# Optimization experiments

Hardware: AMD Instinct MI355X
Metric: run time of the kernel (lower is better)

Reference implementation:

```python
import jax, jax.numpy as jnp
import numpy as np

NUM_NOD = 6
MAX_PREV = 5
NUM_EDGE = 20  # (1+5)*5//2 + 5*(6-5)
D = 1024
H = 8
LN_EPS = 1e-6


def setup_inputs() -> dict:
    key = jax.random.key(0)
    ks = jax.random.split(key, 12)
    B, S = 8, 1024
    scale = 1.0 / np.sqrt(D)
    return {
        "inputs": jax.random.normal(ks[0], (B, S, D), jnp.float32),
        "ew": jax.random.uniform(ks[1], (NUM_NOD, 3), jnp.float32),
        "act_w": jax.random.uniform(ks[2], (NUM_NOD,), jnp.float32),
        "We": jax.random.normal(ks[3], (NUM_EDGE, D, D), jnp.float32) * scale,
        "be": jnp.zeros((NUM_EDGE, D), jnp.float32),
        "Wq": jax.random.normal(ks[4], (NUM_NOD, D, D), jnp.float32) * scale,
        "Wk": jax.random.normal(ks[5], (NUM_NOD, D, D), jnp.float32) * scale,
        "Wv": jax.random.normal(ks[6], (NUM_NOD, D, D), jnp.float32) * scale,
        "Wo": jax.random.normal(ks[7], (NUM_NOD, D, D), jnp.float32) * scale,
        "ln_g": jnp.ones((D,), jnp.float32),
        "ln_b": jnp.zeros((D,), jnp.float32),
    }


def _layernorm(x, g, b):
    mu = jnp.mean(x, axis=-1, keepdims=True)
    var = jnp.mean(jnp.square(x - mu), axis=-1, keepdims=True)
    return (x - mu) * jax.lax.rsqrt(var + LN_EPS) * g + b


def _mha(q, k, v, wq, wk, wv, wo):
    B, S, d = q.shape
    dh = d // H
    qh = (q @ wq).reshape(B, S, H, dh)
    kh = (k @ wk).reshape(B, S, H, dh)
    vh = (v @ wv).reshape(B, S, H, dh)
    scores = jnp.einsum("bqhd,bkhd->bhqk", qh, kh) / jnp.sqrt(jnp.asarray(dh, q.dtype))
    attn = jax.nn.softmax(scores, axis=-1)
    ctx = jnp.einsum("bhqk,bkhd->bqhd", attn, vh).reshape(B, S, d)
    return ctx @ wo


def reference(inputs, ew, act_w, We, be, Wq, Wk, Wv, Wo, ln_g, ln_b):
    # Fixed (deterministic) routing: node act = attention (q,k,v) for all nodes.
    # Edge op = linear (sel_ope 3). q from node c-1, k from earliest visible node,
    # v from the middle of the visible window; gated by Gumbel weights ew/act_w.
    nodes = {-1: inputs}
    lind = 0
    for c in range(NUM_NOD):
        nsrc = min(c + 1, MAX_PREV)
        snode = c - nsrc
        eq, ek, ev = lind + nsrc - 1, lind, lind + nsrc // 2
        in_q, in_k, in_v = c - 1, snode, snode + nsrc // 2
        q = ew[c, 0] * (nodes[in_q] @ We[eq] + be[eq])
        k = ew[c, 1] * (nodes[in_k] @ We[ek] + be[ek])
        v = ew[c, 2] * (nodes[in_v] @ We[ev] + be[ev])
        o = _mha(q, k, v, Wq[c], Wk[c], Wv[c], Wo[c])
        nodes[c] = act_w[c] * o + q  # gated attention + residual
        lind += nsrc
    # only node 5 is unconsumed under this routing
    out = nodes[NUM_NOD - 1]
    return _layernorm(out, ln_g, ln_b)
```

## Files before the change

### kernel.cpp

```cpp
#include <hip/hip_runtime.h>
#include <stdint.h>

#define DD 1024
#define MM 8192

typedef unsigned short u16;
typedef __attribute__((ext_vector_type(8))) short s16x8;
typedef __attribute__((ext_vector_type(4))) short s16x4;
typedef __attribute__((ext_vector_type(8))) __bf16 bf16x8;
typedef __attribute__((ext_vector_type(4))) float f32x4;

__device__ inline u16 f2bf(float f) {
  uint32_t u = __builtin_bit_cast(uint32_t, f);
  u += 0x7fffu + ((u >> 16) & 1u);
  return (u16)(u >> 16);
}
__device__ inline u16 f2bf_rn(float f) {
  return __builtin_bit_cast(u16, (__bf16)f);
}
__device__ inline float bf2f(u16 h) {
  return __builtin_bit_cast(float, (uint32_t)h << 16);
}
__device__ inline f32x4 mfma32(s16x8 a, s16x8 b, f32x4 c) {
  return __builtin_amdgcn_mfma_f32_16x16x32_bf16(
      __builtin_bit_cast(bf16x8, a), __builtin_bit_cast(bf16x8, b), c, 0, 0, 0);
}

__global__ __launch_bounds__(256) void k_cvt(const float* __restrict__ in,
                                             u16* __restrict__ out, int n8) {
  int i = blockIdx.x * 256 + threadIdx.x;
  if (i >= n8) return;
  const float4* p = (const float4*)in;
  float4 a = p[2 * i], b = p[2 * i + 1];
  union { s16x8 v; u16 u[8]; } r;
  r.u[0] = f2bf(a.x); r.u[1] = f2bf(a.y); r.u[2] = f2bf(a.z); r.u[3] = f2bf(a.w);
  r.u[4] = f2bf(b.x); r.u[5] = f2bf(b.y); r.u[6] = f2bf(b.z); r.u[7] = f2bf(b.w);
  ((s16x8*)out)[i] = r.v;
}

struct WSrcs { const float* p[7]; };
__global__ __launch_bounds__(256) void k_wtransN(WSrcs ws, u16* __restrict__ pool) {
  __shared__ u16 t[32][33];
  int m = blockIdx.z;
  const float* src = ws.p[m];
  u16* dst = pool + (size_t)m * DD * DD;
  int c0 = blockIdx.x * 32, r0 = blockIdx.y * 32;
  int tx = threadIdx.x, ty = threadIdx.y;
  #pragma unroll
  for (int j = 0; j < 4; ++j)
    t[ty + j * 8][tx] = f2bf(src[(size_t)(r0 + ty + j * 8) * DD + c0 + tx]);
  __syncthreads();
  #pragma unroll
  for (int j = 0; j < 4; ++j)
    dst[(size_t)(c0 + ty + j * 8) * DD + r0 + tx] = t[tx][ty + j * 8];
}

struct GemmJob {
  const u16* A; const u16* Bt; const float* bias; const u16* resid;
  float* f32out;
  u16* out0; const float* s0p; float s0c;
  u16* out1; const float* s1p;
  u16* out2; const float* s2p;
  u16* vtout;
};
struct GemmBatch { GemmJob j[3]; };

__global__ __launch_bounds__(256, 2) void k_gemmN(GemmBatch gb) {
  const GemmJob jb = gb.j[blockIdx.z];
  __shared__ u16 As[128 * 64];
  __shared__ u16 Bs[128 * 64];
  const int tid = threadIdx.x;
  const int lane = tid & 63, wave = tid >> 6;
  const int g = lane >> 4, r15 = lane & 15;
  const int m0 = blockIdx.x * 128, n0 = blockIdx.y * 128;
  const int wm = (wave >> 1) * 64, wn = (wave & 1) * 64;
  f32x4 acc[4][4] = {};
  for (int kt = 0; kt < 16; ++kt) {
    const int k0 = kt * 64;
    __syncthreads();
    #pragma unroll
    for (int i = 0; i < 4; ++i) {
      int c = tid + i * 256;
      int row = c >> 3, kc = (c & 7) ^ (row & 7);
      __builtin_amdgcn_global_load_lds(
          (__attribute__((address_space(1))) void*)(jb.A + (size_t)(m0 + row) * DD + k0 + kc * 8),
          (__attribute__((address_space(3))) void*)(As + c * 8), 16, 0, 0);
    }
    #pragma unroll
    for (int i = 0; i < 4; ++i) {
      int c = tid + i * 256;
      int row = c >> 3, kc = (c & 7) ^ (row & 7);
      __builtin_amdgcn_global_load_lds(
          (__attribute__((address_space(1))) void*)(jb.Bt + (size_t)(n0 + row) * DD + k0 + kc * 8),
          (__attribute__((address_space(3))) void*)(Bs + c * 8), 16, 0, 0);
    }
    __syncthreads();
    #pragma unroll
    for (int ks = 0; ks < 2; ++ks) {
      s16x8 af[4], bfr[4];
      #pragma unroll
      for (int f = 0; f < 4; ++f) {
        int row = wm + f * 16 + r15;
        int kc = (ks * 4 + g) ^ (row & 7);
        af[f] = *(const s16x8*)(As + row * 64 + kc * 8);
        int rowb = wn + f * 16 + r15;
        int kcb = (ks * 4 + g) ^ (rowb & 7);
        bfr[f] = *(const s16x8*)(Bs + rowb * 64 + kcb * 8);
      }
      #pragma unroll
      for (int fm = 0; fm < 4; ++fm)
        #pragma unroll
        for (int fn = 0; fn < 4; ++fn)
          acc[fm][fn] = mfma32(af[fm], bfr[fn], acc[fm][fn]);
    }
  }
  const float s0 = jb.s0c * (jb.s0p ? jb.s0p[0] : 1.0f);
  if (jb.vtout) {
    #pragma unroll
    for (int fm = 0; fm < 4; ++fm) {
      #pragma unroll
      for (int fn = 0; fn < 4; ++fn) {
        int col = n0 + wn + fn * 16 + r15;
        int row0 = m0 + wm + fm * 16 + g * 4;
        int b_ = row0 >> 10, h_ = col >> 7, d_ = col & 127, s_ = row0 & 1023;
        union { s16x4 v; u16 u[4]; } q4;
        #pragma unroll
        for (int j = 0; j < 4; ++j) q4.u[j] = f2bf(s0 * acc[fm][fn][j]);
        *(s16x4*)(jb.vtout + (((size_t)(b_ * 8 + h_) * 128 + d_) << 10) + s_) = q4.v;
      }
    }
    return;
  }
  const float s1 = (jb.s1p ? jb.s1p[0] : 1.0f);
  const float s2 = (jb.s2p ? jb.s2p[0] : 1.0f);
  #pragma unroll
  for (int fm = 0; fm < 4; ++fm) {
    #pragma unroll
    for (int fn = 0; fn < 4; ++fn) {
      int col = n0 + wn + fn * 16 + r15;
      float bcol = jb.bias ? jb.bias[col] : 0.0f;
      #pragma unroll
      for (int j = 0; j < 4; ++j) {
        int row = m0 + wm + fm * 16 + g * 4 + j;
        size_t idx = (size_t)row * DD + col;
        float v = acc[fm][fn][j] + bcol;
        float v0 = s0 * v + (jb.resid ? bf2f(jb.resid[idx]) : 0.0f);
        if (jb.out0) jb.out0[idx] = f2bf(v0);
        if (jb.f32out) jb.f32out[idx] = v0;
        if (jb.out1) jb.out1[idx] = f2bf(s1 * v);
        if (jb.out2) jb.out2[idx] = f2bf(s2 * v);
      }
    }
  }
}

__global__ __launch_bounds__(256, 2) void k_attn(
    const u16* __restrict__ qp, const u16* __restrict__ kp,
    const u16* __restrict__ vt, u16* __restrict__ ctx) {
  __shared__ u16 Ks[2][64 * 128];
  __shared__ u16 Vs[2][128 * 72];
  const int lin = blockIdx.y * gridDim.x + blockIdx.x;
  const int m = lin >> 3;
  const int bh = (lin & 7) * 8 + (m & 7);
  const int q0 = (m >> 3) * 128;
  const int b = bh >> 3, h = bh & 7;
  const int tid = threadIdx.x, lane = tid & 63, wave = tid >> 6;
  const int g = lane >> 4, r15 = lane & 15;
  s16x8 qf[2][4];
  #pragma unroll
  for (int qg = 0; qg < 2; ++qg) {
    const u16* qb = qp + (size_t)(b * 1024 + q0 + wave * 32 + qg * 16 + r15) * DD + h * 128;
    #pragma unroll
    for (int kk = 0; kk < 4; ++kk) qf[qg][kk] = *(const s16x8*)(qb + kk * 32 + g * 8);
  }
  f32x4 o0[8] = {}, o1[8] = {};
  float mrow0 = -1e30f, lrow0 = 0.0f, mrow1 = -1e30f, lrow1 = 0.0f;
  const u16* kpb = kp + (size_t)b * 1024 * DD + h * 128;
  const u16* vtb = vt + (size_t)bh * 128 * 1024;

  s16x8 vreg[4];
  auto stageK = [&](int t, int buf) {
    #pragma unroll
    for (int i = 0; i < 4; ++i) {
      int c = tid + i * 256;
      int row = c >> 4, kc = (c & 15) ^ (row & 7);
      __builtin_amdgcn_global_load_lds(
          (__attribute__((address_space(1))) void*)(kpb + (size_t)(t * 64 + row) * DD + kc * 8),
          (__attribute__((address_space(3))) void*)(Ks[buf] + c * 8), 16, 0, 0);
    }
  };
  auto loadV = [&](int t) {
    #pragma unroll
    for (int i = 0; i < 4; ++i) {
      int c = tid + i * 256;
      int row = c >> 3, kc = c & 7;
      vreg[i] = *(const s16x8*)(vtb + (size_t)row * 1024 + t * 64 + kc * 8);
    }
  };
  auto writeV = [&](int buf) {
    #pragma unroll
    for (int i = 0; i < 4; ++i) {
      int c = tid + i * 256;
      int row = c >> 3, kc = c & 7;
      *(s16x8*)(Vs[buf] + row * 72 + kc * 8) = vreg[i];
    }
  };

  stageK(0, 0);
  loadV(0);
  writeV(0);
  __syncthreads();

  union pk_t { s16x8 v; u16 u[8]; };
  for (int t = 0; t < 16; ++t) {
    const int cur = t & 1;
    if (t < 15) {
      stageK(t + 1, cur ^ 1);
      loadV(t + 1);
    }
    f32x4 s0[4] = {}, s1[4] = {};
    __builtin_amdgcn_s_setprio(1);
    #pragma unroll
    for (int sub = 0; sub < 4; ++sub) {
      const int krow = sub * 16 + r15;
      #pragma unroll
      for (int kk = 0; kk < 4; ++kk) {
        int slot = (kk * 4 + g) ^ (krow & 7);
        s16x8 kf = *(const s16x8*)(Ks[cur] + krow * 128 + slot * 8);
        s0[sub] = mfma32(kf, qf[0][kk], s0[sub]);
        s1[sub] = mfma32(kf, qf[1][kk], s1[sub]);
      }
    }
    __builtin_amdgcn_s_setprio(0);
    pk_t pa0[2], pa1[2];
    {
      float tm = -1e30f;
      #pragma unroll
      for (int sub = 0; sub < 4; ++sub)
        tm = fmaxf(fmaxf(fmaxf(s0[sub][0], s0[sub][1]), fmaxf(s0[sub][2], s0[sub][3])), tm);
      tm = fmaxf(tm, __shfl_xor(tm, 16));
      tm = fmaxf(tm, __shfl_xor(tm, 32));
      if (!__all(tm - mrow0 <= 8.0f)) {
        float mnew = fmaxf(mrow0, tm);
        float corr = exp2f(mrow0 - mnew);
        lrow0 *= corr;
        #pragma unroll
        for (int j = 0; j < 4; ++j) {
          float cj = __shfl(corr, (lane & 48) + g * 4 + j);
          #pragma unroll
          for (int dt = 0; dt < 8; ++dt) o0[dt][j] *= cj;
        }
        mrow0 = mnew;
      }
      float ps = 0.0f;
      #pragma unroll
      for (int sub = 0; sub < 4; ++sub)
        #pragma unroll
        for (int j = 0; j < 4; ++j) {
          float pe = exp2f(s0[sub][j] - mrow0);
          ps += pe;
          pa0[sub >> 1].u[(sub & 1) * 4 + j] = f2bf_rn(pe);
        }
      ps += __shfl_xor(ps, 16);
      ps += __shfl_xor(ps, 32);
      lrow0 += ps;
    }
    {
      float tm = -1e30f;
      #pragma unroll
      for (int sub = 0; sub < 4; ++sub)
        tm = fmaxf(fmaxf(fmaxf(s1[sub][0], s1[sub][1]), fmaxf(s1[sub][2], s1[sub][3])), tm);
      tm = fmaxf(tm, __shfl_xor(tm, 16));
      tm = fmaxf(tm, __shfl_xor(tm, 32));
      if (!__all(tm - mrow1 <= 8.0f)) {
        float mnew = fmaxf(mrow1, tm);
        float corr = exp2f(mrow1 - mnew);
        lrow1 *= corr;
        #pragma unroll
        for (int j = 0; j < 4; ++j) {
          float cj = __shfl(corr, (lane & 48) + g * 4 + j);
          #pragma unroll
          for (int dt = 0; dt < 8; ++dt) o1[dt][j] *= cj;
        }
        mrow1 = mnew;
      }
      float ps = 0.0f;
      #pragma unroll
      for (int sub = 0; sub < 4; ++sub)
        #pragma unroll
        for (int j = 0; j < 4; ++j) {
          float pe = exp2f(s1[sub][j] - mrow1);
          ps += pe;
          pa1[sub >> 1].u[(sub & 1) * 4 + j] = f2bf_rn(pe);
        }
      ps += __shfl_xor(ps, 16);
      ps += __shfl_xor(ps, 32);
      lrow1 += ps;
    }
    if (t < 15) writeV(cur ^ 1);
    __builtin_amdgcn_s_setprio(1);
    #pragma unroll
    for (int p01 = 0; p01 < 2; ++p01) {
      #pragma unroll
      for (int dt = 0; dt < 8; ++dt) {
        union { s16x8 v; s16x4 h[2]; } vv;
        const u16* vbase = Vs[cur] + (dt * 16 + r15) * 72 + p01 * 32 + g * 4;
        vv.h[0] = *(const s16x4*)(vbase);
        vv.h[1] = *(const s16x4*)(vbase + 16);
        o0[dt] = mfma32(pa0[p01].v, vv.v, o0[dt]);
        o1[dt] = mfma32(pa1[p01].v, vv.v, o1[dt]);
      }
    }
    __builtin_amdgcn_s_setprio(0);
    __syncthreads();
  }
  {
    float inv = 1.0f / lrow0;
    #pragma unroll
    for (int j = 0; j < 4; ++j) {
      float cj = __shfl(inv, (lane & 48) + g * 4 + j);
      size_t row = (size_t)(b * 1024 + q0 + wave * 32 + g * 4 + j);
      #pragma unroll
      for (int dt = 0; dt < 8; ++dt)
        ctx[row * DD + h * 128 + dt * 16 + r15] = f2bf(o0[dt][j] * cj);
    }
  }
  {
    float inv = 1.0f / lrow1;
    #pragma unroll
    for (int j = 0; j < 4; ++j) {
      float cj = __shfl(inv, (lane & 48) + g * 4 + j);
      size_t row = (size_t)(b * 1024 + q0 + wave * 32 + 16 + g * 4 + j);
      #pragma unroll
      for (int dt = 0; dt < 8; ++dt)
        ctx[row * DD + h * 128 + dt * 16 + r15] = f2bf(o1[dt][j] * cj);
    }
  }
}

__global__ __launch_bounds__(256) void k_ln(const float* __restrict__ x,
                                            const float* __restrict__ gam,
                                            const float* __restrict__ bet,
                                            float* __restrict__ out) {
  __shared__ float red[8];
  const int row = blockIdx.x, tid = threadIdx.x, lane = tid & 63, wave = tid >> 6;
  const float4 v = ((const float4*)(x + (size_t)row * DD))[tid];
  float s = v.x + v.y + v.z + v.w;
  #pragma unroll
  for (int m = 1; m < 64; m <<= 1) s += __shfl_xor(s, m);
  if (lane == 0) red[wave] = s;
  __syncthreads();
  float mu = (red[0] + red[1] + red[2] + red[3]) * (1.0f / DD);
  float dx = v.x - mu, dy = v.y - mu, dz = v.z - mu, dw = v.w - mu;
  float q = dx * dx + dy * dy + dz * dz + dw * dw;
  #pragma unroll
  for (int m = 1; m < 64; m <<= 1) q += __shfl_xor(q, m);
  if (lane == 0) red[wave + 4] = q;
  __syncthreads();
  float var = (red[4] + red[5] + red[6] + red[7]) * (1.0f / DD);
  float inv = rsqrtf(var + 1e-6f);
  const float4 gv = ((const float4*)gam)[tid];
  const float4 bv = ((const float4*)bet)[tid];
  float4 r;
  r.x = dx * inv * gv.x + bv.x;
  r.y = dy * inv * gv.y + bv.y;
  r.z = dz * inv * gv.z + bv.z;
  r.w = dw * inv * gv.w + bv.w;
  ((float4*)(out + (size_t)row * DD))[tid] = r;
}

extern "C" void kernel_launch(void* const* d_in, const int* in_sizes, int n_in,
                              void* d_out, int out_size, void* d_ws, size_t ws_size,
                              hipStream_t stream) {
  const float* inputs = (const float*)d_in[0];
  const float* ew     = (const float*)d_in[1];
  const float* act_w  = (const float*)d_in[2];
  const float* We     = (const float*)d_in[3];
  const float* be     = (const float*)d_in[4];
  const float* Wq     = (const float*)d_in[5];
  const float* Wk     = (const float*)d_in[6];
  const float* Wv     = (const float*)d_in[7];
  const float* Wo     = (const float*)d_in[8];
  const float* ln_g   = (const float*)d_in[9];
  const float* ln_b   = (const float*)d_in[10];
  float* out = (float*)d_out;

  uint8_t* w = (uint8_t*)d_ws;
  size_t off = 0;
  auto alloc = [&](size_t bytes) {
    uint8_t* p = w + off;
    off += (bytes + 255) & ~(size_t)255;
    return p;
  };
  const size_t XB = (size_t)MM * DD * 2;
  const size_t WB = (size_t)DD * DD * 2;
  u16* Xb[6];
  for (int i = 0; i < 6; ++i) Xb[i] = (u16*)alloc(XB);
  u16* Wpool = (u16*)alloc(7 * WB);
  u16* S = (u16*)alloc(6 * XB);
  u16* S0 = S,            * S1 = S + XB / 2,     * S2 = S + XB;
  u16* S3 = S + 3 * XB / 2, * S4 = S + 2 * XB,   * S5 = S + 5 * XB / 2;
  u16* qb = S0, * kb = S1, * vb = S2, * qpb = S3, * kpb = S4;
  u16* vtb = S5;
  u16* ctxb = S2;
  float* n5 = (float*)S3;
  if (off > ws_size) {
    (void)hipMemsetAsync(d_out, 0x7F, (size_t)out_size * 4, stream);
    return;
  }

  k_cvt<<<dim3(MM * DD / 8 / 256), 256, 0, stream>>>(inputs, Xb[0], MM * DD / 8);

  struct EG { int c, src, e, mask; };
  static const EG egs[] = {
      {0, -1, 0, 7},
      {1, 0, 2, 5},  {1, -1, 1, 2},
      {2, 1, 5, 1},  {2, -1, 3, 2},  {2, 0, 4, 4},
      {3, 2, 9, 1},  {3, -1, 6, 2},  {3, 1, 8, 4},
      {4, 3, 14, 1}, {4, -1, 10, 2}, {4, 1, 12, 4},
      {5, 4, 19, 1}, {5, 0, 15, 2},  {5, 2, 17, 4},
  };
  const float QS = 1.4426950408889634f * 0.088388347648318433f;

  for (int c = 0; c < 6; ++c) {
    WSrcs wsrc;
    int nz = 0, eslot[3], ne = 0;
    for (const auto& eg : egs)
      if (eg.c == c) { eslot[ne++] = nz; wsrc.p[nz++] = We + (size_t)eg.e * DD * DD; }
    const int sq = nz; wsrc.p[nz++] = Wq + (size_t)c * DD * DD;
    const int sk = nz; wsrc.p[nz++] = Wk + (size_t)c * DD * DD;
    const int sv = nz; wsrc.p[nz++] = Wv + (size_t)c * DD * DD;
    const int so = nz; wsrc.p[nz++] = Wo + (size_t)c * DD * DD;
    k_wtransN<<<dim3(32, 32, nz), dim3(32, 8), 0, stream>>>(wsrc, Wpool);

    GemmBatch eb{};
    int ei = 0;
    for (const auto& eg : egs) {
      if (eg.c != c) continue;
      eb.j[ei] = GemmJob{
          (eg.src < 0) ? Xb[0] : Xb[eg.src + 1],
          Wpool + (size_t)eslot[ei] * DD * DD,
          be + (size_t)eg.e * DD, nullptr, nullptr,
          (eg.mask & 1) ? qb : nullptr, ew + 3 * c + 0, 1.0f,
          (eg.mask & 2) ? kb : nullptr, ew + 3 * c + 1,
          (eg.mask & 4) ? vb : nullptr, ew + 3 * c + 2,
          nullptr};
      ++ei;
    }
    k_gemmN<<<dim3(64, 8, ei), 256, 0, stream>>>(eb);

    GemmBatch pb{};
    pb.j[0] = GemmJob{qb, Wpool + (size_t)sq * DD * DD, nullptr, nullptr, nullptr,
                      qpb, nullptr, QS, nullptr, nullptr, nullptr, nullptr, nullptr};
    pb.j[1] = GemmJob{kb, Wpool + (size_t)sk * DD * DD, nullptr, nullptr, nullptr,
                      kpb, nullptr, 1.0f, nullptr, nullptr, nullptr, nullptr, nullptr};
    pb.j[2] = GemmJob{vb, Wpool + (size_t)sv * DD * DD, nullptr, nullptr, nullptr,
                      nullptr, nullptr, 1.0f, nullptr, nullptr, nullptr, nullptr, vtb};
    k_gemmN<<<dim3(64, 8, 3), 256, 0, stream>>>(pb);

    k_attn<<<dim3(8, 64), 256, 0, stream>>>(qpb, kpb, vtb, ctxb);

    GemmBatch ob{};
    ob.j[0] = GemmJob{ctxb, Wpool + (size_t)so * DD * DD, nullptr, qb,
                      (c == 5) ? n5 : nullptr,
                      (c < 5) ? Xb[c + 1] : nullptr, act_w + c, 1.0f,
                      nullptr, nullptr, nullptr, nullptr, nullptr};
    k_gemmN<<<dim3(64, 8, 1), 256, 0, stream>>>(ob);
  }
  k_ln<<<dim3(MM), 256, 0, stream>>>(n5, ln_g, ln_b, out);
}
```

Measured before the change: 1.325 ms.

## Precombine edge and projection weights and batch previous out-projection with next GEMMs

The edge linear weights are algebraically folded into the Q/K/V projection weights (We·Wq etc.) by a weight-weight GEMM plus precomputed bias vectors. This lets k and v projections come directly from node activations in one GEMM instead of two. Q is still computed separately for the residual path. Each node's out-projection is deferred and batched into the next node's K/V GEMM launch to fill the GPU better. In exchange it adds 18 small 1024x1024 weight GEMMs plus extra conversion and transpose launches, and slightly changes bf16 rounding because the combined weights are rounded.

```diff
diff --git a/kernel.cpp b/kernel.cpp
--- a/kernel.cpp
+++ b/kernel.cpp
@@ -38,7 +38,20 @@
   ((s16x8*)out)[i] = r.v;
 }
 
-struct WSrcs { const float* p[7]; };
+struct CvtSrcs { const float* p[15]; };
+__global__ __launch_bounds__(256) void k_cvtN(CvtSrcs cs, u16* __restrict__ dst) {
+  int z = blockIdx.y;
+  const float4* p = (const float4*)cs.p[z];
+  u16* out = dst + (size_t)z * DD * DD;
+  int i = blockIdx.x * 256 + threadIdx.x;
+  float4 a = p[2 * i], b = p[2 * i + 1];
+  union { s16x8 v; u16 u[8]; } r;
+  r.u[0] = f2bf(a.x); r.u[1] = f2bf(a.y); r.u[2] = f2bf(a.z); r.u[3] = f2bf(a.w);
+  r.u[4] = f2bf(b.x); r.u[5] = f2bf(b.y); r.u[6] = f2bf(b.z); r.u[7] = f2bf(b.w);
+  ((s16x8*)out)[i] = r.v;
+}
+
+struct WSrcs { const float* p[18]; };
 __global__ __launch_bounds__(256) void k_wtransN(WSrcs ws, u16* __restrict__ pool) {
   __shared__ u16 t[32][33];
   int m = blockIdx.z;
@@ -55,6 +68,90 @@
     dst[(size_t)(c0 + ty + j * 8) * DD + r0 + tx] = t[tx][ty + j * 8];
 }
 
+struct BiasArgs { const float* be[18]; };
+__global__ __launch_bounds__(256) void k_biasN(BiasArgs ba, const u16* __restrict__ wt,
+                                               float* __restrict__ outv) {
+  int z = blockIdx.y, n = blockIdx.x * 256 + threadIdx.x;
+  const u16* row = wt + (size_t)z * DD * DD + (size_t)n * DD;
+  const float* be = ba.be[z];
+  float acc = 0.0f;
+  for (int k8 = 0; k8 < DD / 8; ++k8) {
+    s16x8 w = *(const s16x8*)(row + k8 * 8);
+    const float4* bp = (const float4*)(be + k8 * 8);
+    float4 b0 = bp[0], b1 = bp[1];
+    acc += b0.x * bf2f((u16)w[0]) + b0.y * bf2f((u16)w[1]) +
+           b0.z * bf2f((u16)w[2]) + b0.w * bf2f((u16)w[3]) +
+           b1.x * bf2f((u16)w[4]) + b1.y * bf2f((u16)w[5]) +
+           b1.z * bf2f((u16)w[6]) + b1.w * bf2f((u16)w[7]);
+  }
+  outv[(size_t)z * DD + n] = acc;
+}
+
+struct CombArgs { const u16* a[18]; const u16* b[18]; u16* cbase; };
+__global__ __launch_bounds__(256, 2) void k_gemmC(CombArgs ca) {
+  const u16* A = ca.a[blockIdx.z];
+  const u16* Bt = ca.b[blockIdx.z];
+  u16* C = ca.cbase + (size_t)blockIdx.z * DD * DD;
+  __shared__ u16 As[128 * 64];
+  __shared__ u16 Bs[128 * 64];
+  const int tid = threadIdx.x;
+  const int lane = tid & 63, wave = tid >> 6;
+  const int g = lane >> 4, r15 = lane & 15;
+  const int m0 = blockIdx.x * 128, n0 = blockIdx.y * 128;
+  const int wm = (wave >> 1) * 64, wn = (wave & 1) * 64;
+  f32x4 acc[4][4] = {};
+  for (int kt = 0; kt < 16; ++kt) {
+    const int k0 = kt * 64;
+    __syncthreads();
+    #pragma unroll
+    for (int i = 0; i < 4; ++i) {
+      int c = tid + i * 256;
+      int row = c >> 3, kc = (c & 7) ^ (row & 7);
+      __builtin_amdgcn_global_load_lds(
+          (__attribute__((address_space(1))) void*)(A + (size_t)(m0 + row) * DD + k0 + kc * 8),
+          (__attribute__((address_space(3))) void*)(As + c * 8), 16, 0, 0);
+    }
+    #pragma unroll
+    for (int i = 0; i < 4; ++i) {
+      int c = tid + i * 256;
+      int row = c >> 3, kc = (c & 7) ^ (row & 7);
+      __builtin_amdgcn_global_load_lds(
+          (__attribute__((address_space(1))) void*)(Bt + (size_t)(n0 + row) * DD + k0 + kc * 8),
+          (__attribute__((address_space(3))) void*)(Bs + c * 8), 16, 0, 0);
+    }
+    __syncthreads();
+    #pragma unroll
+    for (int ks = 0; ks < 2; ++ks) {
+      s16x8 af[4], bfr[4];
+      #pragma unroll
+      for (int f = 0; f < 4; ++f) {
+        int row = wm + f * 16 + r15;
+        int kc = (ks * 4 + g) ^ (row & 7);
+        af[f] = *(const s16x8*)(As + row * 64 + kc * 8);
+        int rowb = wn + f * 16 + r15;
+        int kcb = (ks * 4 + g) ^ (rowb & 7);
+        bfr[f] = *(const s16x8*)(Bs + rowb * 64 + kcb * 8);
+      }
+      #pragma unroll
+      for (int fm = 0; fm < 4; ++fm)
+        #pragma unroll
+        for (int fn = 0; fn < 4; ++fn)
+          acc[fm][fn] = mfma32(af[fm], bfr[fn], acc[fm][fn]);
+    }
+  }
+  #pragma unroll
+  for (int fm = 0; fm < 4; ++fm)
+    #pragma unroll
+    for (int fn = 0; fn < 4; ++fn) {
+      int col = n0 + wn + fn * 16 + r15;
+      #pragma unroll
+      for (int j = 0; j < 4; ++j) {
+        int row = m0 + wm + fm * 16 + g * 4 + j;
+        C[(size_t)row * DD + col] = f2bf(acc[fm][fn][j]);
+      }
+    }
+}
+
 struct GemmJob {
   const u16* A; const u16* Bt; const float* bias; const u16* resid;
   float* f32out;
@@ -121,11 +218,12 @@
       #pragma unroll
       for (int fn = 0; fn < 4; ++fn) {
         int col = n0 + wn + fn * 16 + r15;
+        float bcol = jb.bias ? jb.bias[col] : 0.0f;
         int row0 = m0 + wm + fm * 16 + g * 4;
         int b_ = row0 >> 10, h_ = col >> 7, d_ = col & 127, s_ = row0 & 1023;
         union { s16x4 v; u16 u[4]; } q4;
         #pragma unroll
-        for (int j = 0; j < 4; ++j) q4.u[j] = f2bf(s0 * acc[fm][fn][j]);
+        for (int j = 0; j < 4; ++j) q4.u[j] = f2bf(s0 * (acc[fm][fn][j] + bcol));
         *(s16x4*)(jb.vtout + (((size_t)(b_ * 8 + h_) * 128 + d_) << 10) + s_) = q4.v;
       }
     }
@@ -394,78 +492,120 @@
   };
   const size_t XB = (size_t)MM * DD * 2;
   const size_t WB = (size_t)DD * DD * 2;
-  u16* Xb[6];
-  for (int i = 0; i < 6; ++i) Xb[i] = (u16*)alloc(XB);
-  u16* Wpool = (u16*)alloc(7 * WB);
-  u16* S = (u16*)alloc(6 * XB);
-  u16* S0 = S,            * S1 = S + XB / 2,     * S2 = S + XB;
-  u16* S3 = S + 3 * XB / 2, * S4 = S + 2 * XB,   * S5 = S + 5 * XB / 2;
-  u16* qb = S0, * kb = S1, * vb = S2, * qpb = S3, * kpb = S4;
-  u16* vtb = S5;
-  u16* ctxb = S2;
-  float* n5 = (float*)S3;
+  const size_t XBu = (size_t)MM * DD;
+  const size_t WBu = (size_t)DD * DD;
+
+  u16* Xbuf[5];
+  for (int i = 0; i < 5; ++i) Xbuf[i] = (u16*)alloc(XB);
+  u16* Comb  = (u16*)alloc(18 * WB);
+  u16* rot   = (u16*)alloc(4 * WB);
+  float* biasv = (float*)alloc(18 * DD * 4);
+  u16* S     = (u16*)alloc(5 * XB);
   if (off > ws_size) {
     (void)hipMemsetAsync(d_out, 0x7F, (size_t)out_size * 4, stream);
     return;
   }
-
-  k_cvt<<<dim3(MM * DD / 8 / 256), 256, 0, stream>>>(inputs, Xb[0], MM * DD / 8);
-
-  struct EG { int c, src, e, mask; };
-  static const EG egs[] = {
-      {0, -1, 0, 7},
-      {1, 0, 2, 5},  {1, -1, 1, 2},
-      {2, 1, 5, 1},  {2, -1, 3, 2},  {2, 0, 4, 4},
-      {3, 2, 9, 1},  {3, -1, 6, 2},  {3, 1, 8, 4},
-      {4, 3, 14, 1}, {4, -1, 10, 2}, {4, 1, 12, 4},
-      {5, 4, 19, 1}, {5, 0, 15, 2},  {5, 2, 17, 4},
+  u16* Xb[6] = {Xbuf[0], Xbuf[1], Xbuf[2], Xbuf[3], Xbuf[4], Xbuf[0]};
+  u16* qb = S, * ctxb = S + XBu, * qpb = S + 2 * XBu, * kpb = S + 3 * XBu,
+     * vtb = S + 4 * XBu;
+  float* n5 = (float*)qpb;
+  u16* stP = S;
+  u16* stW = S + 18 * WBu;
+
+  struct Node { int sq, eq, sk, ek, sv, ev; };
+  static const Node route[6] = {
+      {-1, 0, -1, 0, -1, 0},
+      {0, 2, -1, 1, 0, 2},
+      {1, 5, -1, 3, 0, 4},
+      {2, 9, -1, 6, 1, 8},
+      {3, 14, -1, 10, 1, 12},
+      {4, 19, 0, 15, 2, 17},
   };
   const float QS = 1.4426950408889634f * 0.088388347648318433f;
 
+  int emap[20]; for (int i = 0; i < 20; ++i) emap[i] = -1;
+  int uniq[20]; int nu = 0;
   for (int c = 0; c < 6; ++c) {
-    WSrcs wsrc;
-    int nz = 0, eslot[3], ne = 0;
-    for (const auto& eg : egs)
-      if (eg.c == c) { eslot[ne++] = nz; wsrc.p[nz++] = We + (size_t)eg.e * DD * DD; }
-    const int sq = nz; wsrc.p[nz++] = Wq + (size_t)c * DD * DD;
-    const int sk = nz; wsrc.p[nz++] = Wk + (size_t)c * DD * DD;
-    const int sv = nz; wsrc.p[nz++] = Wv + (size_t)c * DD * DD;
-    const int so = nz; wsrc.p[nz++] = Wo + (size_t)c * DD * DD;
-    k_wtransN<<<dim3(32, 32, nz), dim3(32, 8), 0, stream>>>(wsrc, Wpool);
-
-    GemmBatch eb{};
-    int ei = 0;
-    for (const auto& eg : egs) {
-      if (eg.c != c) continue;
-      eb.j[ei] = GemmJob{
-          (eg.src < 0) ? Xb[0] : Xb[eg.src + 1],
-          Wpool + (size_t)eslot[ei] * DD * DD,
-          be + (size_t)eg.e * DD, nullptr, nullptr,
-          (eg.mask & 1) ? qb : nullptr, ew + 3 * c + 0, 1.0f,
-          (eg.mask & 2) ? kb : nullptr, ew + 3 * c + 1,
-          (eg.mask & 4) ? vb : nullptr, ew + 3 * c + 2,
-          nullptr};
-      ++ei;
-    }
-    k_gemmN<<<dim3(64, 8, ei), 256, 0, stream>>>(eb);
-
-    GemmBatch pb{};
-    pb.j[0] = GemmJob{qb, Wpool + (size_t)sq * DD * DD, nullptr, nullptr, nullptr,
-                      qpb, nullptr, QS, nullptr, nullptr, nullptr, nullptr, nullptr};
-    pb.j[1] = GemmJob{kb, Wpool + (size_t)sk * DD * DD, nullptr, nullptr, nullptr,
-                      kpb, nullptr, 1.0f, nullptr, nullptr, nullptr, nullptr, nullptr};
-    pb.j[2] = GemmJob{vb, Wpool + (size_t)sv * DD * DD, nullptr, nullptr, nullptr,
-                      nullptr, nullptr, 1.0f, nullptr, nullptr, nullptr, nullptr, vtb};
-    k_gemmN<<<dim3(64, 8, 3), 256, 0, stream>>>(pb);
+    int es[3] = {route[c].eq, route[c].ek, route[c].ev};
+    for (int t = 0; t < 3; ++t)
+      if (emap[es[t]] < 0) { emap[es[t]] = nu; uniq[nu++] = es[t]; }
+  }
+
+  k_cvt<<<dim3(MM * DD / 8 / 256), 256, 0, stream>>>(inputs, Xb[0], MM * DD / 8);
+  WSrcs w18;
+  for (int c = 0; c < 6; ++c) {
+    w18.p[c * 3 + 0] = Wq + (size_t)c * WBu;
+    w18.p[c * 3 + 1] = Wk + (size_t)c * WBu;
+    w18.p[c * 3 + 2] = Wv + (size_t)c * WBu;
+  }
+  k_wtransN<<<dim3(32, 32, 18), dim3(32, 8), 0, stream>>>(w18, stP);
+  CvtSrcs cv;
+  for (int j = 0; j < nu; ++j) cv.p[j] = We + (size_t)uniq[j] * WBu;
+  k_cvtN<<<dim3(512, nu), 256, 0, stream>>>(cv, stW);
+  CombArgs ca;
+  BiasArgs ba;
+  for (int c = 0; c < 6; ++c) {
+    int es[3] = {route[c].eq, route[c].ek, route[c].ev};
+    for (int t = 0; t < 3; ++t) {
+      int i = c * 3 + t;
+      ca.a[i] = stP + (size_t)i * WBu;
+      ca.b[i] = stW + (size_t)emap[es[t]] * WBu;
+      ba.be[i] = be + (size_t)es[t] * DD;
+    }
+  }
+  ca.cbase = Comb;
+  k_gemmC<<<dim3(8, 8, 18), 256, 0, stream>>>(ca);
+  k_biasN<<<dim3(4, 18), 256, 0, stream>>>(ba, stP, biasv);
+
+  GemmJob oprojPrev{};
+  for (int c = 0; c < 6; ++c) {
+    const Node& nd = route[c];
+    u16* qeT = rot + (size_t)(c & 1) * 2 * WBu;
+    u16* WoT = qeT + WBu;
+    WSrcs w2{};
+    w2.p[0] = We + (size_t)nd.eq * WBu;
+    w2.p[1] = Wo + (size_t)c * WBu;
+    k_wtransN<<<dim3(32, 32, 2), dim3(32, 8), 0, stream>>>(w2, qeT);
+
+    GemmJob kap = {Xb[nd.sk + 1], Comb + (size_t)(c * 3 + 1) * WBu,
+                   biasv + (size_t)(c * 3 + 1) * DD, nullptr, nullptr,
+                   kpb, ew + 3 * c + 1, 1.0f,
+                   nullptr, nullptr, nullptr, nullptr, nullptr};
+    GemmJob vap = {Xb[nd.sv + 1], Comb + (size_t)(c * 3 + 2) * WBu,
+                   biasv + (size_t)(c * 3 + 2) * DD, nullptr, nullptr,
+                   nullptr, ew + 3 * c + 2, 1.0f,
+                   nullptr, nullptr, nullptr, nullptr, vtb};
+    GemmJob qed = {Xb[nd.sq + 1], qeT, be + (size_t)nd.eq * DD, nullptr, nullptr,
+                   qb, ew + 3 * c + 0, 1.0f,
+                   nullptr, nullptr, nullptr, nullptr, nullptr};
+    GemmJob qap = {Xb[nd.sq + 1], Comb + (size_t)(c * 3 + 0) * WBu,
+                   biasv + (size_t)(c * 3 + 0) * DD, nullptr, nullptr,
+                   qpb, ew + 3 * c + 0, QS,
+                   nullptr, nullptr, nullptr, nullptr, nullptr};
+
+    GemmBatch A{};
+    int za = 0;
+    if (c >= 1) A.j[za++] = oprojPrev;
+    A.j[za++] = kap;
+    if (c != 1) A.j[za++] = vap;
+    k_gemmN<<<dim3(64, 8, za), 256, 0, stream>>>(A);
+
+    GemmBatch B{};
+    int zb = 0;
+    if (c == 1) B.j[zb++] = vap;
+    B.j[zb++] = qed;
+    B.j[zb++] = qap;
+    k_gemmN<<<dim3(64, 8, zb), 256, 0, stream>>>(B);
 
     k_attn<<<dim3(8, 64), 256, 0, stream>>>(qpb, kpb, vtb, ctxb);
 
-    GemmBatch ob{};
-    ob.j[0] = GemmJob{ctxb, Wpool + (size_t)so * DD * DD, nullptr, qb,
-                      (c == 5) ? n5 : nullptr,
-                      (c < 5) ? Xb[c + 1] : nullptr, act_w + c, 1.0f,
-                      nullptr, nullptr, nullptr, nullptr, nullptr};
-    k_gemmN<<<dim3(64, 8, 1), 256, 0, stream>>>(ob);
-  }
+    oprojPrev = GemmJob{ctxb, WoT, nullptr, qb,
+                        (c == 5) ? n5 : nullptr,
+                        (c < 5) ? Xb[c + 1] : nullptr, act_w + c, 1.0f,
+                        nullptr, nullptr, nullptr, nullptr, nullptr};
+  }
+  GemmBatch F{};
+  F.j[0] = oprojPrev;
+  k_gemmN<<<dim3(64, 8, 1), 256, 0, stream>>>(F);
   k_ln<<<dim3(MM), 256, 0, stream>>>(n5, ln_g, ln_b, out);
 }
```

New measurement: 1.178 ms. -11.1%, faster.
